# Optimization experiments

Hardware: AMD Instinct MI355X
Metric: run time of the kernel (lower is better)

The kernel has to match this reference:

```python
import jax, jax.numpy as jnp
import numpy as np

N_WIRES = 4
DEPTH = 2
N_PATCH = 196  # 14*14 2x2 patches of a 28x28 image


def _ry(state, theta, w):
    """Apply RY(theta) on wire w. state: [B,P,2,2,2,2]; theta: scalar or [B,P]."""
    ax = 2 + w
    half = theta * 0.5
    c = jnp.cos(half)
    s = jnp.sin(half)
    # broadcast angle over remaining wire axes
    c = c.reshape(c.shape + (1,) * (state.ndim - 1 - c.ndim))
    s = s.reshape(s.shape + (1,) * (state.ndim - 1 - s.ndim))
    s0 = jnp.take(state, 0, axis=ax)
    s1 = jnp.take(state, 1, axis=ax)
    return jnp.stack([c * s0 - s * s1, s * s0 + c * s1], axis=ax)


def _cnot(state, cw, tw):
    """CNOT with control wire cw, target wire tw."""
    ca, ta = 2 + cw, 2 + tw
    c0 = jnp.take(state, 0, axis=ca)
    c1 = jnp.take(state, 1, axis=ca)
    ta_adj = ta - 1 if ta > ca else ta  # axis shift after take along ca
    return jnp.stack([c0, jnp.flip(c1, axis=ta_adj)], axis=ca)


def _quanv_features(x, var_angles):
    """Batched exact 4-qubit state-vector sim over all 196 patches at once."""
    B = x.shape[0]
    img = x.reshape(B, 28, 28)
    # [B,14,2,14,2] -> [B,14,14,2,2] -> [B,196,4]: (r,c),(r,c+1),(r+1,c),(r+1,c+1)
    patches = img.reshape(B, 14, 2, 14, 2).transpose(0, 1, 3, 2, 4).reshape(B, N_PATCH, 4)
    # RY/CNOT circuit keeps amplitudes real -> real fp32 state [B,P,2,2,2,2]
    state = jnp.zeros((B, N_PATCH, 2, 2, 2, 2), dtype=x.dtype)
    state = state.at[:, :, 0, 0, 0, 0].set(1.0)
    # encoder: RY(pixel) on each wire
    for w in range(N_WIRES):
        state = _ry(state, patches[:, :, w], w)
    # variational layer: per depth, learnable RY on each wire + CNOT ring
    for d in range(DEPTH):
        for w in range(N_WIRES):
            state = _ry(state, var_angles[d, w], w)
        for cw in range(N_WIRES):
            state = _cnot(state, cw, (cw + 1) % N_WIRES)
    probs = state * state
    # <Z_w> = P(wire w = 0) - P(wire w = 1)
    feats = jnp.stack(
        [(jnp.take(probs, 0, axis=2 + w) - jnp.take(probs, 1, axis=2 + w)).sum(axis=(2, 3, 4))
         for w in range(N_WIRES)], axis=-1)  # [B,196,4]
    return feats.reshape(B, N_PATCH * N_WIRES)  # [B,784]


def setup_inputs() -> dict:
    key = jax.random.key(0)
    k1, k2, k3, k4 = jax.random.split(key, 4)
    B = 4096
    x = jax.random.uniform(k1, (B, 1, 28, 28), dtype=jnp.float32)  # pixel-like angles
    var_angles = jax.random.normal(k2, (DEPTH, N_WIRES), dtype=jnp.float32)
    W1 = jax.random.normal(k3, (256, 784), dtype=jnp.float32) * (1.0 / np.sqrt(784.0))
    b1 = jnp.zeros((256,), dtype=jnp.float32)
    W2 = jax.random.normal(k4, (10, 256), dtype=jnp.float32) * (1.0 / np.sqrt(256.0))
    b2 = jnp.zeros((10,), dtype=jnp.float32)
    return {"x": x, "var_angles": var_angles, "W1": W1, "b1": b1, "W2": W2, "b2": b2}


def reference(x, var_angles, W1, b1, W2, b2):
    feats = _quanv_features(x, var_angles)            # [B,784]
    h = jax.nn.relu(feats @ W1.T + b1)                # dropout is identity in eval
    logits = h @ W2.T + b2                            # [B,10]
    return jax.nn.log_softmax(logits, axis=-1)
```

## Files before the change

### kernel.cpp

```cpp
#include <hip/hip_runtime.h>
#include <math.h>

typedef short bf16x8 __attribute__((ext_vector_type(8)));
typedef float f32x4 __attribute__((ext_vector_type(4)));

#define KP 800
#define AS_LD 808
#define HS_LD 260

__device__ __forceinline__ unsigned short f2bf(float f) {
    unsigned int u = __float_as_uint(f);
    u = (u + 0x7FFFu + ((u >> 16) & 1u)) >> 16;
    return (unsigned short)u;
}

__global__ __launch_bounds__(256) void w1cvt_kernel(
        const float* __restrict__ W1, unsigned short* __restrict__ w1bf) {
    const int id = blockIdx.x * 256 + threadIdx.x;
    const int r = id / KP;
    const int c = id - r * KP;
    w1bf[id] = f2bf((c < 784) ? W1[r * 784 + c] : 0.f);
}


__device__ __forceinline__ void ry_gate(float a[16], int bitpos, float c, float s) {
    const int mask = 1 << bitpos;
#pragma unroll
    for (int i = 0; i < 16; ++i) {
        if (!(i & mask)) {
            const int j = i | mask;
            const float a0 = a[i], a1 = a[j];
            a[i] = c * a0 - s * a1;
            a[j] = s * a0 + c * a1;
        }
    }
}

__device__ __forceinline__ void cnot_gate(float a[16], int cbit, int tbit) {
    const int cmask = 1 << cbit, tmask = 1 << tbit;
#pragma unroll
    for (int i = 0; i < 16; ++i) {
        if ((i & cmask) && !(i & tmask)) {
            const int j = i | tmask;
            const float tmp = a[i];
            a[i] = a[j];
            a[j] = tmp;
        }
    }
}

__global__ __launch_bounds__(512) void fused_kernel(
        const float* __restrict__ x, const float* __restrict__ var_angles,
        const unsigned short* __restrict__ w1bf, const float* __restrict__ b1,
        const float* __restrict__ W2, const float* __restrict__ b2,
        float* __restrict__ out) {
    __shared__ unsigned short As[16][AS_LD];
    __shared__ float Hs[16][HS_LD];
    __shared__ float W2s[2560];
    __shared__ float b1s[256];
    __shared__ float b2s[12];

    const int tid = threadIdx.x;
    const int r0 = blockIdx.x * 16;

#pragma unroll
    for (int i = tid; i < 2560; i += 512) W2s[i] = W2[i];
    if (tid < 256) b1s[tid] = b1[tid];
    if (tid < 10) b2s[tid] = b2[tid];

    if (tid < 64) {
        const ushort4 zz = {0, 0, 0, 0};
        *(ushort4*)&As[tid >> 2][784 + (tid & 3) * 4] = zz;
    }

    float vvc[8], vvs[8];
#pragma unroll
    for (int i = 0; i < 8; ++i) {
        const float h = 0.5f * var_angles[i];
        vvs[i] = __sinf(h);
        vvc[i] = __cosf(h);
    }

    for (int i = tid; i < 16 * 196; i += 512) {
        const int lr = i / 196;
        const int p = i - lr * 196;
        const int pr = p / 14;
        const int pc = p - pr * 14;

        const float* img = x + (size_t)(r0 + lr) * 784;
        const float2 top = *(const float2*)(img + (2 * pr) * 28 + 2 * pc);
        const float2 bot = *(const float2*)(img + (2 * pr + 1) * 28 + 2 * pc);
        const float theta[4] = {top.x, top.y, bot.x, bot.y};

        float c[4], s[4];
#pragma unroll
        for (int w = 0; w < 4; ++w) {
            const float h = 0.5f * theta[w];
            s[w] = __sinf(h);
            c[w] = __cosf(h);
        }

        float a[16];
#pragma unroll
        for (int k = 0; k < 16; ++k) {
            float v = (k & 8) ? s[0] : c[0];
            v *= (k & 4) ? s[1] : c[1];
            v *= (k & 2) ? s[2] : c[2];
            v *= (k & 1) ? s[3] : c[3];
            a[k] = v;
        }

#pragma unroll
        for (int d = 0; d < 2; ++d) {
#pragma unroll
            for (int w = 0; w < 4; ++w)
                ry_gate(a, 3 - w, vvc[d * 4 + w], vvs[d * 4 + w]);
            cnot_gate(a, 3, 2);
            cnot_gate(a, 2, 1);
            cnot_gate(a, 1, 0);
            cnot_gate(a, 0, 3);
        }

        float z[4] = {0.f, 0.f, 0.f, 0.f};
#pragma unroll
        for (int k = 0; k < 16; ++k) {
            const float pr2 = a[k] * a[k];
            z[0] += (k & 8) ? -pr2 : pr2;
            z[1] += (k & 4) ? -pr2 : pr2;
            z[2] += (k & 2) ? -pr2 : pr2;
            z[3] += (k & 1) ? -pr2 : pr2;
        }

        ushort4 hv;
        unsigned short* hp = (unsigned short*)&hv;
#pragma unroll
        for (int w = 0; w < 4; ++w) hp[w] = f2bf(z[w]);
        *(ushort4*)&As[lr][p * 4] = hv;
    }
    __syncthreads();

    const int lane = tid & 63;
    const int wv = tid >> 6;
    const int q = lane >> 4;
    const int lm = lane & 15;
    const int n0 = wv * 32;

    const unsigned short* pB0 = w1bf + (size_t)(n0 + lm) * KP + q * 8;
    const unsigned short* pB1 = pB0 + (size_t)16 * KP;

    f32x4 acc0 = (f32x4)(0.f), acc1 = (f32x4)(0.f);

    bf16x8 b0a = *(const bf16x8*)(pB0);
    bf16x8 b1a = *(const bf16x8*)(pB1);
    bf16x8 b0b = *(const bf16x8*)(pB0 + 32);
    bf16x8 b1b = *(const bf16x8*)(pB1 + 32);

    for (int k0 = 0; k0 < KP; k0 += 32) {
        const bf16x8 a = *(const bf16x8*)&As[lm][k0 + q * 8];
        acc0 = __builtin_amdgcn_mfma_f32_16x16x32_bf16(a, b0a, acc0, 0, 0, 0);
        acc1 = __builtin_amdgcn_mfma_f32_16x16x32_bf16(a, b1a, acc1, 0, 0, 0);
        b0a = b0b;
        b1a = b1b;
        if (k0 + 64 < KP) {
            b0b = *(const bf16x8*)(pB0 + k0 + 64);
            b1b = *(const bf16x8*)(pB1 + k0 + 64);
        }
    }

    const float bias0 = b1s[n0 + lm];
    const float bias1 = b1s[n0 + 16 + lm];
#pragma unroll
    for (int i = 0; i < 4; ++i) {
        const int r = q * 4 + i;
        Hs[r][n0 + lm]      = fmaxf(acc0[i] + bias0, 0.f);
        Hs[r][n0 + 16 + lm] = fmaxf(acc1[i] + bias1, 0.f);
    }
    __syncthreads();

    const int er = tid >> 5;
    const int el = tid & 31;

    const float4 h0 = *(const float4*)&Hs[er][el * 8];
    const float4 h1 = *(const float4*)&Hs[er][el * 8 + 4];

    float part[10];
#pragma unroll
    for (int j = 0; j < 10; ++j) {
        const float4 w0 = *(const float4*)&W2s[j * 256 + el * 8];
        const float4 w1 = *(const float4*)&W2s[j * 256 + el * 8 + 4];
        part[j] = h0.x * w0.x + h0.y * w0.y + h0.z * w0.z + h0.w * w0.w +
                  h1.x * w1.x + h1.y * w1.y + h1.z * w1.z + h1.w * w1.w;
    }
#pragma unroll
    for (int mask = 1; mask < 32; mask <<= 1) {
#pragma unroll
        for (int j = 0; j < 10; ++j) part[j] += __shfl_xor(part[j], mask, 64);
    }

    float lg[10];
#pragma unroll
    for (int j = 0; j < 10; ++j) lg[j] = part[j] + b2s[j];
    float m = lg[0];
#pragma unroll
    for (int j = 1; j < 10; ++j) m = fmaxf(m, lg[j]);
    float se = 0.f;
#pragma unroll
    for (int j = 0; j < 10; ++j) se += expf(lg[j] - m);
    const float lse = m + logf(se);

    if (el < 10) out[(size_t)(r0 + er) * 10 + el] = lg[el] - lse;
}


extern "C" void kernel_launch(void* const* d_in, const int* in_sizes, int n_in,
                              void* d_out, int out_size, void* d_ws, size_t ws_size,
                              hipStream_t stream) {
    const float* x   = (const float*)d_in[0];
    const float* var = (const float*)d_in[1];
    const float* W1  = (const float*)d_in[2];
    const float* b1  = (const float*)d_in[3];
    const float* W2  = (const float*)d_in[4];
    const float* b2  = (const float*)d_in[5];
    float* out = (float*)d_out;

    const int B = in_sizes[0] / 784;

    unsigned short* w1bf = (unsigned short*)d_ws;

    w1cvt_kernel<<<(256 * KP) / 256, 256, 0, stream>>>(W1, w1bf);
    fused_kernel<<<B / 16, 512, 0, stream>>>(x, var, w1bf, b1, W2, b2, out);
}
```

Measured before the change: 90.19 us.

## Double block size to 1024 threads, prefetch pixels, simplify quantum sim math

```diff
diff --git a/kernel.cpp b/kernel.cpp
--- a/kernel.cpp
+++ b/kernel.cpp
@@ -49,7 +49,7 @@
     }
 }
 
-__global__ __launch_bounds__(512) void fused_kernel(
+__global__ __launch_bounds__(1024) void fused_kernel(
         const float* __restrict__ x, const float* __restrict__ var_angles,
         const unsigned short* __restrict__ w1bf, const float* __restrict__ b1,
         const float* __restrict__ W2, const float* __restrict__ b2,
@@ -63,8 +63,7 @@
     const int tid = threadIdx.x;
     const int r0 = blockIdx.x * 16;
 
-#pragma unroll
-    for (int i = tid; i < 2560; i += 512) W2s[i] = W2[i];
+    for (int idx = tid; idx < 2560; idx += 1024) W2s[idx] = W2[idx];
     if (tid < 256) b1s[tid] = b1[tid];
     if (tid < 10) b2s[tid] = b2[tid];
 
@@ -75,40 +74,50 @@
 
     float vvc[8], vvs[8];
 #pragma unroll
-    for (int i = 0; i < 8; ++i) {
-        const float h = 0.5f * var_angles[i];
-        vvs[i] = __sinf(h);
-        vvc[i] = __cosf(h);
-    }
-
-    for (int i = tid; i < 16 * 196; i += 512) {
+    for (int ii = 0; ii < 8; ++ii) {
+        const float h = 0.5f * var_angles[ii];
+        vvs[ii] = __sinf(h);
+        vvc[ii] = __cosf(h);
+    }
+
+#define PIXLOAD(II, T, B) { \
+        const int lr_ = (II) / 196; \
+        const int p_  = (II) - lr_ * 196; \
+        const int pr_ = p_ / 14; \
+        const int pc_ = p_ - pr_ * 14; \
+        const float* img_ = x + (size_t)(r0 + lr_) * 784 + (2 * pr_) * 28 + 2 * pc_; \
+        T = *(const float2*)(img_); \
+        B = *(const float2*)(img_ + 28); \
+    }
+
+    int i = tid;
+    float2 top, bot;
+    PIXLOAD(i, top, bot)
+    for (;;) {
+        const int inxt = i + 1024;
+        const bool more = (inxt < 16 * 196);
+        float2 topn, botn;
+        if (more) PIXLOAD(inxt, topn, botn)
+
         const int lr = i / 196;
-        const int p = i - lr * 196;
-        const int pr = p / 14;
-        const int pc = p - pr * 14;
-
-        const float* img = x + (size_t)(r0 + lr) * 784;
-        const float2 top = *(const float2*)(img + (2 * pr) * 28 + 2 * pc);
-        const float2 bot = *(const float2*)(img + (2 * pr + 1) * 28 + 2 * pc);
-        const float theta[4] = {top.x, top.y, bot.x, bot.y};
+        const int p  = i - lr * 196;
 
         float c[4], s[4];
-#pragma unroll
-        for (int w = 0; w < 4; ++w) {
-            const float h = 0.5f * theta[w];
-            s[w] = __sinf(h);
-            c[w] = __cosf(h);
-        }
-
+        {
+            const float th[4] = {top.x, top.y, bot.x, bot.y};
+#pragma unroll
+            for (int w = 0; w < 4; ++w) {
+                const float h = 0.5f * th[w];
+                s[w] = __sinf(h);
+                c[w] = __cosf(h);
+            }
+        }
+
+        const float p01[4] = {c[0] * c[1], c[0] * s[1], s[0] * c[1], s[0] * s[1]};
+        const float p23[4] = {c[2] * c[3], c[2] * s[3], s[2] * c[3], s[2] * s[3]};
         float a[16];
 #pragma unroll
-        for (int k = 0; k < 16; ++k) {
-            float v = (k & 8) ? s[0] : c[0];
-            v *= (k & 4) ? s[1] : c[1];
-            v *= (k & 2) ? s[2] : c[2];
-            v *= (k & 1) ? s[3] : c[3];
-            a[k] = v;
-        }
+        for (int k = 0; k < 16; ++k) a[k] = p01[k >> 2] * p23[k & 3];
 
 #pragma unroll
         for (int d = 0; d < 2; ++d) {
@@ -121,21 +130,31 @@
             cnot_gate(a, 0, 3);
         }
 
-        float z[4] = {0.f, 0.f, 0.f, 0.f};
+        float S0 = 0.f, S1 = 0.f, S2 = 0.f, S3 = 0.f;
 #pragma unroll
         for (int k = 0; k < 16; ++k) {
-            const float pr2 = a[k] * a[k];
-            z[0] += (k & 8) ? -pr2 : pr2;
-            z[1] += (k & 4) ? -pr2 : pr2;
-            z[2] += (k & 2) ? -pr2 : pr2;
-            z[3] += (k & 1) ? -pr2 : pr2;
-        }
-
-        ushort4 hv;
-        unsigned short* hp = (unsigned short*)&hv;
-#pragma unroll
-        for (int w = 0; w < 4; ++w) hp[w] = f2bf(z[w]);
-        *(ushort4*)&As[lr][p * 4] = hv;
+            if (!(k & 8)) S0 = __builtin_fmaf(a[k], a[k], S0);
+            if (!(k & 4)) S1 = __builtin_fmaf(a[k], a[k], S1);
+            if (!(k & 2)) S2 = __builtin_fmaf(a[k], a[k], S2);
+            if (!(k & 1)) S3 = __builtin_fmaf(a[k], a[k], S3);
+        }
+        const float z0 = __builtin_fmaf(2.f, S0, -1.f);
+        const float z1 = __builtin_fmaf(2.f, S1, -1.f);
+        const float z2 = __builtin_fmaf(2.f, S2, -1.f);
+        const float z3 = __builtin_fmaf(2.f, S3, -1.f);
+
+        unsigned int lo, hi;
+        asm("v_cvt_pk_bf16_f32 %0, %1, %2" : "=v"(lo) : "v"(z0), "v"(z1));
+        asm("v_cvt_pk_bf16_f32 %0, %1, %2" : "=v"(hi) : "v"(z2), "v"(z3));
+        uint2 hv;
+        hv.x = lo;
+        hv.y = hi;
+        *(uint2*)&As[lr][p * 4] = hv;
+
+        if (!more) break;
+        i = inxt;
+        top = topn;
+        bot = botn;
     }
     __syncthreads();
 
@@ -143,56 +162,43 @@
     const int wv = tid >> 6;
     const int q = lane >> 4;
     const int lm = lane & 15;
-    const int n0 = wv * 32;
-
-    const unsigned short* pB0 = w1bf + (size_t)(n0 + lm) * KP + q * 8;
-    const unsigned short* pB1 = pB0 + (size_t)16 * KP;
-
-    f32x4 acc0 = (f32x4)(0.f), acc1 = (f32x4)(0.f);
-
-    bf16x8 b0a = *(const bf16x8*)(pB0);
-    bf16x8 b1a = *(const bf16x8*)(pB1);
-    bf16x8 b0b = *(const bf16x8*)(pB0 + 32);
-    bf16x8 b1b = *(const bf16x8*)(pB1 + 32);
+    const int n0 = wv * 16;
+
+    const unsigned short* pB = w1bf + (size_t)(n0 + lm) * KP + q * 8;
+
+    f32x4 acc = (f32x4)(0.f);
+    bf16x8 bcur = *(const bf16x8*)(pB);
+    bf16x8 bnxt = *(const bf16x8*)(pB + 32);
 
     for (int k0 = 0; k0 < KP; k0 += 32) {
-        const bf16x8 a = *(const bf16x8*)&As[lm][k0 + q * 8];
-        acc0 = __builtin_amdgcn_mfma_f32_16x16x32_bf16(a, b0a, acc0, 0, 0, 0);
-        acc1 = __builtin_amdgcn_mfma_f32_16x16x32_bf16(a, b1a, acc1, 0, 0, 0);
-        b0a = b0b;
-        b1a = b1b;
+        const bf16x8 afrag = *(const bf16x8*)&As[lm][k0 + q * 8];
+        acc = __builtin_amdgcn_mfma_f32_16x16x32_bf16(afrag, bcur, acc, 0, 0, 0);
+        bcur = bnxt;
         if (k0 + 64 < KP) {
-            b0b = *(const bf16x8*)(pB0 + k0 + 64);
-            b1b = *(const bf16x8*)(pB1 + k0 + 64);
-        }
-    }
-
-    const float bias0 = b1s[n0 + lm];
-    const float bias1 = b1s[n0 + 16 + lm];
-#pragma unroll
-    for (int i = 0; i < 4; ++i) {
-        const int r = q * 4 + i;
-        Hs[r][n0 + lm]      = fmaxf(acc0[i] + bias0, 0.f);
-        Hs[r][n0 + 16 + lm] = fmaxf(acc1[i] + bias1, 0.f);
+            bnxt = *(const bf16x8*)(pB + k0 + 64);
+        }
+    }
+
+    const float bias = b1s[n0 + lm];
+#pragma unroll
+    for (int ii = 0; ii < 4; ++ii) {
+        Hs[q * 4 + ii][n0 + lm] = fmaxf(acc[ii] + bias, 0.f);
     }
     __syncthreads();
 
-    const int er = tid >> 5;
-    const int el = tid & 31;
-
-    const float4 h0 = *(const float4*)&Hs[er][el * 8];
-    const float4 h1 = *(const float4*)&Hs[er][el * 8 + 4];
+    const int er = tid >> 6;
+    const int el = tid & 63;
+
+    const float4 h = *(const float4*)&Hs[er][el * 4];
 
     float part[10];
 #pragma unroll
     for (int j = 0; j < 10; ++j) {
-        const float4 w0 = *(const float4*)&W2s[j * 256 + el * 8];
-        const float4 w1 = *(const float4*)&W2s[j * 256 + el * 8 + 4];
-        part[j] = h0.x * w0.x + h0.y * w0.y + h0.z * w0.z + h0.w * w0.w +
-                  h1.x * w1.x + h1.y * w1.y + h1.z * w1.z + h1.w * w1.w;
-    }
-#pragma unroll
-    for (int mask = 1; mask < 32; mask <<= 1) {
+        const float4 w = *(const float4*)&W2s[j * 256 + el * 4];
+        part[j] = h.x * w.x + h.y * w.y + h.z * w.z + h.w * w.w;
+    }
+#pragma unroll
+    for (int mask = 1; mask < 64; mask <<= 1) {
 #pragma unroll
         for (int j = 0; j < 10; ++j) part[j] += __shfl_xor(part[j], mask, 64);
     }
@@ -228,5 +234,5 @@
     unsigned short* w1bf = (unsigned short*)d_ws;
 
     w1cvt_kernel<<<(256 * KP) / 256, 256, 0, stream>>>(W1, w1bf);
-    fused_kernel<<<B / 16, 512, 0, stream>>>(x, var, w1bf, b1, W2, b2, out);
-}
+    fused_kernel<<<B / 16, 1024, 0, stream>>>(x, var, w1bf, b1, W2, b2, out);
+}
```

Result: faster. 87.49 us (-3.0%).
